# Kernel optimization log

Hardware: AMD Instinct MI355X
Metric: run time of the kernel (lower is better)

Reference implementation:

```python
import jax, jax.numpy as jnp
import numpy as np

N_NODES = 100000
N_EDGES = 1600000
D = 128
NUM_GRAPHS = 256


def setup_inputs() -> dict:
    key = jax.random.key(0)
    ks = jax.random.split(key, 8)
    x = jax.random.normal(ks[0], (N_NODES, D), dtype=jnp.float32)
    edge_index = jax.random.randint(ks[1], (2, N_EDGES), 0, N_NODES, dtype=jnp.int32)
    edge_attr = jax.random.normal(ks[2], (N_EDGES, D), dtype=jnp.float32) * 0.1
    batch = jnp.sort(jax.random.randint(ks[3], (N_NODES,), 0, NUM_GRAPHS, dtype=jnp.int32))
    primary = jax.random.randint(ks[4], (N_NODES,), 0, 2, dtype=jnp.int32)  # 1=primary, 0=condition
    scale = 1.0 / np.sqrt(D)
    W1 = jax.random.normal(ks[5], (D, D), dtype=jnp.float32) * scale
    b1 = jnp.zeros((D,), dtype=jnp.float32)
    W2 = jax.random.normal(ks[6], (D, D), dtype=jnp.float32) * scale
    b2 = jnp.zeros((D,), dtype=jnp.float32)
    return {"x": x, "edge_index": edge_index, "edge_attr": edge_attr,
            "batch": batch, "primary": primary,
            "W1": W1, "b1": b1, "W2": W2, "b2": b2}


def reference(x, edge_index, edge_attr, batch, primary, W1, b1, W2, b2):
    n = x.shape[0]
    # --- GIN-style GNN layer: node_rep = MLP(x + sum_{e:(s->d)} (x[s] + e_attr)) ---
    src, dst = edge_index[0], edge_index[1]
    msg = x[src] + edge_attr                                  # [E, D] gather (memory-bound)
    agg = jax.ops.segment_sum(msg, dst, num_segments=n)       # [N, D] scatter-add
    h = jax.nn.relu((x + agg) @ W1 + b1) @ W2 + b2            # [N, D]

    # --- per-graph mean pool over condition nodes (primary == 0) ---
    cond = (primary == 0)
    condf = cond.astype(h.dtype)[:, None]
    csum = jax.ops.segment_sum(h * condf, batch, num_segments=NUM_GRAPHS)   # [G, D]
    ccnt = jax.ops.segment_sum(condf, batch, num_segments=NUM_GRAPHS)       # [G, 1]
    # graphs with no condition nodes get a zero pool (matches torch branch)
    pool = jnp.where(ccnt > 0, csum / jnp.maximum(ccnt, 1.0), 0.0)          # [G, D]

    # --- assemble rows: per graph, primary rows [h | cond_pool] first, then zero rows
    # for condition nodes (matches the torch concat order) ---
    key = batch * 2 + cond.astype(batch.dtype)      # primary nodes sort before condition nodes
    order = jnp.argsort(key, stable=True)
    h_o = h[order]                                   # [N, D]
    pool_o = pool[batch[order]]                      # [N, D]
    prim_o = (primary[order] == 1)[:, None]
    out = jnp.where(prim_o, jnp.concatenate([h_o, pool_o], axis=1), 0.0)    # [N, 2D]
    return out
```

## Files before the change

kernel.cpp:

```cpp
#include <hip/hip_runtime.h>

#define D 128
#define NG 256

typedef __attribute__((ext_vector_type(8))) short bf16x8;
typedef __attribute__((ext_vector_type(4))) float f32x4;
typedef __attribute__((ext_vector_type(4))) float f4;
typedef __attribute__((ext_vector_type(2))) int i2;
typedef __attribute__((ext_vector_type(4))) ushort u16x4;

__device__ inline ushort f2bf(float f) {
  uint b = __float_as_uint(f);
  return (ushort)((b + 0x7fffu + ((b >> 16) & 1u)) >> 16);
}
__device__ inline float bf2f(ushort u) { return __uint_as_float((uint)u << 16); }

__global__ __launch_bounds__(256) void deg_counts_kernel(const int* __restrict__ ei,
                                                         int* __restrict__ deg,
                                                         const int* __restrict__ batch,
                                                         const int* __restrict__ primary,
                                                         int* __restrict__ ncount,
                                                         int* __restrict__ ccnt, int E, int N) {
  int e = blockIdx.x * blockDim.x + threadIdx.x;
  if (e < E) {
    int d = __builtin_nontemporal_load(&ei[E + e]);
    atomicAdd(&deg[d], 1);
  }
  if (e < N) {
    int g = batch[e];
    atomicAdd(&ncount[g], 1);
    if (primary[e] == 0) atomicAdd(&ccnt[g], 1);
  }
}

__global__ __launch_bounds__(256) void scan_block_sums(const int* __restrict__ deg,
                                                       int* __restrict__ bsum, int N) {
  __shared__ int red[256];
  int t = threadIdx.x;
  int base = blockIdx.x * 1024;
  int s = 0;
#pragma unroll
  for (int j = 0; j < 4; ++j) {
    int i = base + t * 4 + j;
    if (i < N) s += deg[i];
  }
  red[t] = s;
  __syncthreads();
  for (int o = 128; o > 0; o >>= 1) {
    if (t < o) red[t] += red[t + o];
    __syncthreads();
  }
  if (t == 0) bsum[blockIdx.x] = red[0];
}

__global__ void scan_bsum(int* __restrict__ bsum, int nb) {
  if (threadIdx.x == 0) {
    int run = 0;
    for (int i = 0; i < nb; ++i) {
      int v = bsum[i];
      bsum[i] = run;
      run += v;
    }
  }
}

__global__ __launch_bounds__(256) void scan_final(const int* __restrict__ deg,
                                                  const int* __restrict__ bsum,
                                                  int* __restrict__ off, int N) {
  __shared__ int ts[256];
  int t = threadIdx.x;
  int base = blockIdx.x * 1024;
  int v[4];
  int s = 0;
#pragma unroll
  for (int j = 0; j < 4; ++j) {
    int i = base + t * 4 + j;
    v[j] = (i < N) ? deg[i] : 0;
    s += v[j];
  }
  ts[t] = s;
  __syncthreads();
  for (int o = 1; o < 256; o <<= 1) {
    int u = (t >= o) ? ts[t - o] : 0;
    __syncthreads();
    ts[t] += u;
    __syncthreads();
  }
  int excl = ts[t] - s + bsum[blockIdx.x];
#pragma unroll
  for (int j = 0; j < 4; ++j) {
    int i = base + t * 4 + j;
    if (i < N) off[i] = excl;
    excl += v[j];
    if (i == N - 1) off[N] = excl;
  }
}

__global__ __launch_bounds__(256) void fill_kernel(const int* __restrict__ ei,
                                                   const int* __restrict__ off,
                                                   int* __restrict__ cursor,
                                                   i2* __restrict__ csr, int E) {
  int e = blockIdx.x * blockDim.x + threadIdx.x;
  if (e >= E) return;
  int s = __builtin_nontemporal_load(&ei[e]);
  int d = __builtin_nontemporal_load(&ei[E + e]);
  int slot = atomicAdd(&cursor[d], 1);
  i2 v;
  v.x = s;
  v.y = e;
  __builtin_nontemporal_store(v, &csr[off[d] + slot]);
}

__global__ __launch_bounds__(256) void cvt_kernel(const float* __restrict__ x,
                                                  ushort* __restrict__ xb,
                                                  const float* __restrict__ W1,
                                                  const float* __restrict__ W2,
                                                  ushort* __restrict__ W1T,
                                                  ushort* __restrict__ W2T, int total4) {
  int i = blockIdx.x * blockDim.x + threadIdx.x;
  if (i < total4) {
    f4 v = __builtin_nontemporal_load(&((const f4*)x)[i]);
    u16x4 o;
    o.x = f2bf(v.x);
    o.y = f2bf(v.y);
    o.z = f2bf(v.z);
    o.w = f2bf(v.w);
    ((u16x4*)xb)[i] = o;
  }
  if (i < 2 * D * D) {
    int w = i >> 14;
    int k = (i >> 7) & 127;
    int n = i & 127;
    const float* src = w ? W2 : W1;
    ushort* dst = w ? W2T : W1T;
    dst[n * 128 + k] = f2bf(src[k * 128 + n]);
  }
}

__global__ __launch_bounds__(256) void gather_kernel(const ushort* __restrict__ xb,
                                                     const float* __restrict__ ea,
                                                     const i2* __restrict__ csr,
                                                     const int* __restrict__ off,
                                                     ushort* __restrict__ yb, int N) {
  long long tid = (long long)blockIdx.x * blockDim.x + threadIdx.x;
  int n = (int)(tid >> 5);
  int c = (int)(tid & 31);
  if (n >= N) return;
  const f4* ea4 = (const f4*)ea;
  const u16x4* xb4 = (const u16x4*)xb;
  u16x4 self = xb4[(size_t)n * 32 + c];
  f4 acc;
  acc.x = bf2f(self.x);
  acc.y = bf2f(self.y);
  acc.z = bf2f(self.z);
  acc.w = bf2f(self.w);
  int s = off[n], e = off[n + 1];
  int k = s;
  for (; k + 4 <= e; k += 4) {
    i2 p0 = __builtin_nontemporal_load(&csr[k]);
    i2 p1 = __builtin_nontemporal_load(&csr[k + 1]);
    i2 p2 = __builtin_nontemporal_load(&csr[k + 2]);
    i2 p3 = __builtin_nontemporal_load(&csr[k + 3]);
    f4 a0 = __builtin_nontemporal_load(&ea4[(size_t)p0.y * 32 + c]);
    f4 a1 = __builtin_nontemporal_load(&ea4[(size_t)p1.y * 32 + c]);
    f4 a2 = __builtin_nontemporal_load(&ea4[(size_t)p2.y * 32 + c]);
    f4 a3 = __builtin_nontemporal_load(&ea4[(size_t)p3.y * 32 + c]);
    u16x4 u0 = xb4[(size_t)p0.x * 32 + c];
    u16x4 u1 = xb4[(size_t)p1.x * 32 + c];
    u16x4 u2 = xb4[(size_t)p2.x * 32 + c];
    u16x4 u3 = xb4[(size_t)p3.x * 32 + c];
    acc.x += (a0.x + bf2f(u0.x)) + (a1.x + bf2f(u1.x));
    acc.y += (a0.y + bf2f(u0.y)) + (a1.y + bf2f(u1.y));
    acc.z += (a0.z + bf2f(u0.z)) + (a1.z + bf2f(u1.z));
    acc.w += (a0.w + bf2f(u0.w)) + (a1.w + bf2f(u1.w));
    acc.x += (a2.x + bf2f(u2.x)) + (a3.x + bf2f(u3.x));
    acc.y += (a2.y + bf2f(u2.y)) + (a3.y + bf2f(u3.y));
    acc.z += (a2.z + bf2f(u2.z)) + (a3.z + bf2f(u3.z));
    acc.w += (a2.w + bf2f(u2.w)) + (a3.w + bf2f(u3.w));
  }
  for (; k < e; ++k) {
    i2 p0 = __builtin_nontemporal_load(&csr[k]);
    f4 a0 = __builtin_nontemporal_load(&ea4[(size_t)p0.y * 32 + c]);
    u16x4 u0 = xb4[(size_t)p0.x * 32 + c];
    acc.x += a0.x + bf2f(u0.x);
    acc.y += a0.y + bf2f(u0.y);
    acc.z += a0.z + bf2f(u0.z);
    acc.w += a0.w + bf2f(u0.w);
  }
  u16x4 o;
  o.x = f2bf(acc.x);
  o.y = f2bf(acc.y);
  o.z = f2bf(acc.z);
  o.w = f2bf(acc.w);
  __builtin_nontemporal_store(o, &((u16x4*)yb)[(size_t)n * 32 + c]);
}

__global__ void scan_kernel(const int* __restrict__ ncount, int* __restrict__ gstart) {
  __shared__ int a[NG];
  int tx = threadIdx.x;
  int v = ncount[tx];
  a[tx] = v;
  __syncthreads();
  for (int off = 1; off < NG; off <<= 1) {
    int u = (tx >= off) ? a[tx - off] : 0;
    __syncthreads();
    a[tx] += u;
    __syncthreads();
  }
  gstart[tx] = a[tx] - v;
  if (tx == NG - 1) gstart[NG] = a[tx];
}

__global__ __launch_bounds__(256) void rank_kernel(const int* __restrict__ primary,
                                                   const int* __restrict__ gstart,
                                                   const int* __restrict__ ccnt,
                                                   int* __restrict__ pos) {
  int g = blockIdx.x;
  int s = gstart[g], e = gstart[g + 1];
  int pcnt = (e - s) - ccnt[g];
  __shared__ int wcntP[4], wcntC[4];
  int prun = 0, crun = 0;
  for (int i0 = s; i0 < e; i0 += 256) {
    int n = i0 + threadIdx.x;
    bool valid = n < e;
    int isP = (valid && primary[n] == 1) ? 1 : 0;
    int isC = (valid && primary[n] != 1) ? 1 : 0;
    unsigned long long mP = __ballot(isP);
    unsigned long long mC = __ballot(isC);
    int lane = threadIdx.x & 63;
    int wid = threadIdx.x >> 6;
    if (lane == 0) { wcntP[wid] = __popcll(mP); wcntC[wid] = __popcll(mC); }
    __syncthreads();
    int preP = __popcll(mP & ((1ULL << lane) - 1ULL));
    int preC = __popcll(mC & ((1ULL << lane) - 1ULL));
    int woffP = 0, woffC = 0;
#pragma unroll
    for (int ww = 0; ww < 4; ++ww)
      if (ww < wid) { woffP += wcntP[ww]; woffC += wcntC[ww]; }
    int totP = wcntP[0] + wcntP[1] + wcntP[2] + wcntP[3];
    int totC = wcntC[0] + wcntC[1] + wcntC[2] + wcntC[3];
    if (valid) {
      if (isP)
        pos[n] = s + prun + woffP + preP;
      else
        pos[n] = ~(s + pcnt + crun + woffC + preC);
    }
    prun += totP;
    crun += totC;
    __syncthreads();
  }
}

__global__ __launch_bounds__(256) void mlp_mfma_kernel(
    const ushort* __restrict__ yb, float* __restrict__ out,
    const ushort* __restrict__ W1T, const float* __restrict__ b1,
    const ushort* __restrict__ W2T, const float* __restrict__ b2,
    const int* __restrict__ batch, const int* __restrict__ primary,
    const int* __restrict__ pos, float* __restrict__ csum, int N) {
  __shared__ ushort tl[4][16][D];
  __shared__ float csl[4][D];
  const int tid = threadIdx.x;
  const int w = tid >> 6;
  const int l = tid & 63;
  const int lr = l & 15;
  const int lg = l >> 4;
  const int base = blockIdx.x * 64;
  const int m0 = base + w * 16;

  for (int i = tid; i < 4 * D; i += 256) ((float*)csl)[i] = 0.f;
  int gmin = batch[base < N ? base : N - 1];
  __syncthreads();

  f32x4 acc[8];
#pragma unroll
  for (int t = 0; t < 8; ++t) {
    float bv = b1[t * 16 + lr];
    acc[t][0] = bv; acc[t][1] = bv; acc[t][2] = bv; acc[t][3] = bv;
  }
  int arow = m0 + lr;
  if (arow >= N) arow = N - 1;
#pragma unroll
  for (int kk = 0; kk < 4; ++kk) {
    bf16x8 a = *(const bf16x8*)&yb[(size_t)arow * D + kk * 32 + lg * 8];
#pragma unroll
    for (int t = 0; t < 8; ++t) {
      bf16x8 b = *(const bf16x8*)&W1T[(size_t)(t * 16 + lr) * D + kk * 32 + lg * 8];
      acc[t] = __builtin_amdgcn_mfma_f32_16x16x32_bf16(a, b, acc[t], 0, 0, 0);
    }
  }
#pragma unroll
  for (int t = 0; t < 8; ++t) {
#pragma unroll
    for (int r = 0; r < 4; ++r) {
      float v = acc[t][r];
      v = v > 0.f ? v : 0.f;
      int m = lg * 4 + r;
      int col = (t * 16 + lr) ^ ((m & 7) << 3);
      tl[w][m][col] = f2bf(v);
    }
  }
  __syncthreads();

  f32x4 acc2[8];
#pragma unroll
  for (int t = 0; t < 8; ++t) {
    float bv = b2[t * 16 + lr];
    acc2[t][0] = bv; acc2[t][1] = bv; acc2[t][2] = bv; acc2[t][3] = bv;
  }
#pragma unroll
  for (int kk = 0; kk < 4; ++kk) {
    bf16x8 a = *(const bf16x8*)&tl[w][lr][(kk * 32 + lg * 8) ^ ((lr & 7) << 3)];
#pragma unroll
    for (int t = 0; t < 8; ++t) {
      bf16x8 b = *(const bf16x8*)&W2T[(size_t)(t * 16 + lr) * D + kk * 32 + lg * 8];
      acc2[t] = __builtin_amdgcn_mfma_f32_16x16x32_bf16(a, b, acc2[t], 0, 0, 0);
    }
  }

#pragma unroll
  for (int r = 0; r < 4; ++r) {
    int m = m0 + lg * 4 + r;
    if (m >= N) continue;
    int p = pos[m];
    if (p >= 0) {
      size_t ro = (size_t)p * 256;
#pragma unroll
      for (int t = 0; t < 8; ++t)
        __builtin_nontemporal_store(acc2[t][r], &out[ro + t * 16 + lr]);
    } else {
      size_t ro = (size_t)(~p) * 256;
#pragma unroll
      for (int t = 0; t < 8; ++t) {
        __builtin_nontemporal_store(0.0f, &out[ro + t * 16 + lr]);
        __builtin_nontemporal_store(0.0f, &out[ro + 128 + t * 16 + lr]);
      }
      int g = batch[m];
      int gl = g - gmin;
      if (gl < 4) {
#pragma unroll
        for (int t = 0; t < 8; ++t) atomicAdd(&csl[gl][t * 16 + lr], acc2[t][r]);
      } else {
#pragma unroll
        for (int t = 0; t < 8; ++t)
          unsafeAtomicAdd(&csum[(size_t)g * D + t * 16 + lr], acc2[t][r]);
      }
    }
  }
  __syncthreads();
  for (int i = tid; i < 4 * D; i += 256) {
    float v = ((float*)csl)[i];
    if (v != 0.f) {
      int gl = i >> 7, c = i & 127;
      unsafeAtomicAdd(&csum[(size_t)(gmin + gl) * D + c], v);
    }
  }
}

__global__ __launch_bounds__(256) void poolwrite_kernel(const float* __restrict__ csum,
                                                        const int* __restrict__ ccnt,
                                                        const int* __restrict__ batch,
                                                        const int* __restrict__ pos,
                                                        float* __restrict__ out, int N) {
  long long tid = (long long)blockIdx.x * blockDim.x + threadIdx.x;
  int n = (int)(tid >> 5);
  int c = (int)(tid & 31);
  if (n >= N) return;
  int p = pos[n];
  if (p < 0) return;
  int g = batch[n];
  int cnt = ccnt[g];
  f4 v = {0.f, 0.f, 0.f, 0.f};
  if (cnt > 0) {
    f4 s4 = ((const f4*)csum)[(size_t)g * 32 + c];
    float inv = 1.0f / (float)cnt;
    v = s4 * inv;
  }
  __builtin_nontemporal_store(v, &((f4*)out)[(size_t)p * 64 + 32 + c]);
}

extern "C" void kernel_launch(void* const* d_in, const int* in_sizes, int n_in,
                              void* d_out, int out_size, void* d_ws, size_t ws_size,
                              hipStream_t stream) {
  const float* x = (const float*)d_in[0];
  const int* ei = (const int*)d_in[1];
  const float* ea = (const float*)d_in[2];
  const int* batch = (const int*)d_in[3];
  const int* primary = (const int*)d_in[4];
  const float* W1 = (const float*)d_in[5];
  const float* b1 = (const float*)d_in[6];
  const float* W2 = (const float*)d_in[7];
  const float* b2 = (const float*)d_in[8];
  float* out = (float*)d_out;

  const int N = in_sizes[0] / D;
  const int E = in_sizes[1] / 2;
  const int nb = (N + 1023) / 1024;

  float* csum = (float*)d_ws;
  ushort* yb = (ushort*)(csum + (size_t)NG * D);
  ushort* xb = yb + (size_t)N * D;
  ushort* W1T = xb + (size_t)N * D;
  ushort* W2T = W1T + D * D;
  i2* csr = (i2*)(W2T + D * D);
  int* ip = (int*)(csr + (size_t)E);
  int* deg = ip;
  int* off = deg + N;
  int* cursor = off + N + 4;
  int* bsum = cursor + N;
  int* ccnt = bsum + 128;
  int* ncount = ccnt + NG;
  int* gstart = ncount + NG;
  int* pos = gstart + 260;

  hipMemsetAsync(csum, 0, (size_t)NG * D * 4, stream);
  hipMemsetAsync(deg, 0, (size_t)N * 4, stream);
  hipMemsetAsync(cursor, 0, (size_t)N * 4, stream);
  hipMemsetAsync(ccnt, 0, (size_t)NG * 2 * 4, stream);

  deg_counts_kernel<<<(E + 255) / 256, 256, 0, stream>>>(ei, deg, batch, primary, ncount, ccnt,
                                                         E, N);
  scan_block_sums<<<nb, 256, 0, stream>>>(deg, bsum, N);
  scan_bsum<<<1, 64, 0, stream>>>(bsum, nb);
  scan_final<<<nb, 256, 0, stream>>>(deg, bsum, off, N);
  fill_kernel<<<(E + 255) / 256, 256, 0, stream>>>(ei, off, cursor, csr, E);
  cvt_kernel<<<((N * D / 4) + 255) / 256, 256, 0, stream>>>(x, xb, W1, W2, W1T, W2T, N * D / 4);
  {
    long long threads = (long long)N * 32;
    gather_kernel<<<(int)((threads + 255) / 256), 256, 0, stream>>>(xb, ea, csr, off, yb, N);
  }
  scan_kernel<<<1, NG, 0, stream>>>(ncount, gstart);
  rank_kernel<<<NG, 256, 0, stream>>>(primary, gstart, ccnt, pos);
  mlp_mfma_kernel<<<(N + 63) / 64, 256, 0, stream>>>(yb, out, W1T, b1, W2T, b2, batch, primary,
                                                     pos, csum, N);
  poolwrite_kernel<<<(int)(((long long)N * 32 + 255) / 256), 256, 0, stream>>>(csum, ccnt, batch,
                                                                               pos, out, N);
}
```

Before: 648.2 us.

## Fuse prep kernels, parallelize block-sum scan, split edge gather across half-waves

```diff
diff --git a/kernel.cpp b/kernel.cpp
--- a/kernel.cpp
+++ b/kernel.cpp
@@ -15,21 +15,33 @@
 }
 __device__ inline float bf2f(ushort u) { return __uint_as_float((uint)u << 16); }
 
-__global__ __launch_bounds__(256) void deg_counts_kernel(const int* __restrict__ ei,
-                                                         int* __restrict__ deg,
-                                                         const int* __restrict__ batch,
-                                                         const int* __restrict__ primary,
-                                                         int* __restrict__ ncount,
-                                                         int* __restrict__ ccnt, int E, int N) {
-  int e = blockIdx.x * blockDim.x + threadIdx.x;
-  if (e < E) {
-    int d = __builtin_nontemporal_load(&ei[E + e]);
-    atomicAdd(&deg[d], 1);
-  }
-  if (e < N) {
-    int g = batch[e];
+__global__ __launch_bounds__(256) void prep_kernel(
+    const int* __restrict__ ei, int* __restrict__ deg,
+    const int* __restrict__ batch, const int* __restrict__ primary,
+    int* __restrict__ ncount, int* __restrict__ ccnt,
+    const float* __restrict__ x, ushort* __restrict__ xb,
+    const float* __restrict__ W1, const float* __restrict__ W2,
+    ushort* __restrict__ W1T, ushort* __restrict__ W2T, int E, int N, int total4) {
+  int i = blockIdx.x * blockDim.x + threadIdx.x;
+  if (i < E) atomicAdd(&deg[ei[E + i]], 1);
+  if (i < N) {
+    int g = batch[i];
     atomicAdd(&ncount[g], 1);
-    if (primary[e] == 0) atomicAdd(&ccnt[g], 1);
+    if (primary[i] == 0) atomicAdd(&ccnt[g], 1);
+  }
+  if (i < total4) {
+    f4 v = __builtin_nontemporal_load(&((const f4*)x)[i]);
+    u16x4 o;
+    o.x = f2bf(v.x); o.y = f2bf(v.y); o.z = f2bf(v.z); o.w = f2bf(v.w);
+    ((u16x4*)xb)[i] = o;
+  }
+  if (i < 2 * D * D) {
+    int w = i >> 14;
+    int k = (i >> 7) & 127;
+    int n = i & 127;
+    const float* src = w ? W2 : W1;
+    ushort* dst = w ? W2T : W1T;
+    dst[n * 128 + k] = f2bf(src[k * 128 + n]);
   }
 }
 
@@ -54,14 +66,18 @@
 }
 
 __global__ void scan_bsum(int* __restrict__ bsum, int nb) {
-  if (threadIdx.x == 0) {
-    int run = 0;
-    for (int i = 0; i < nb; ++i) {
-      int v = bsum[i];
-      bsum[i] = run;
-      run += v;
-    }
-  }
+  __shared__ int a[128];
+  int t = threadIdx.x;
+  int v = (t < nb) ? bsum[t] : 0;
+  a[t] = v;
+  __syncthreads();
+  for (int o = 1; o < 128; o <<= 1) {
+    int u = (t >= o) ? a[t - o] : 0;
+    __syncthreads();
+    a[t] += u;
+    __syncthreads();
+  }
+  if (t < nb) bsum[t] = a[t] - v;
 }
 
 __global__ __launch_bounds__(256) void scan_final(const int* __restrict__ deg,
@@ -102,97 +118,91 @@
                                                    i2* __restrict__ csr, int E) {
   int e = blockIdx.x * blockDim.x + threadIdx.x;
   if (e >= E) return;
-  int s = __builtin_nontemporal_load(&ei[e]);
-  int d = __builtin_nontemporal_load(&ei[E + e]);
+  int s = ei[e];
+  int d = ei[E + e];
   int slot = atomicAdd(&cursor[d], 1);
   i2 v;
   v.x = s;
   v.y = e;
-  __builtin_nontemporal_store(v, &csr[off[d] + slot]);
-}
-
-__global__ __launch_bounds__(256) void cvt_kernel(const float* __restrict__ x,
-                                                  ushort* __restrict__ xb,
-                                                  const float* __restrict__ W1,
-                                                  const float* __restrict__ W2,
-                                                  ushort* __restrict__ W1T,
-                                                  ushort* __restrict__ W2T, int total4) {
-  int i = blockIdx.x * blockDim.x + threadIdx.x;
-  if (i < total4) {
-    f4 v = __builtin_nontemporal_load(&((const f4*)x)[i]);
-    u16x4 o;
-    o.x = f2bf(v.x);
-    o.y = f2bf(v.y);
-    o.z = f2bf(v.z);
-    o.w = f2bf(v.w);
-    ((u16x4*)xb)[i] = o;
-  }
-  if (i < 2 * D * D) {
-    int w = i >> 14;
-    int k = (i >> 7) & 127;
-    int n = i & 127;
-    const float* src = w ? W2 : W1;
-    ushort* dst = w ? W2T : W1T;
-    dst[n * 128 + k] = f2bf(src[k * 128 + n]);
-  }
-}
-
-__global__ __launch_bounds__(256) void gather_kernel(const ushort* __restrict__ xb,
-                                                     const float* __restrict__ ea,
-                                                     const i2* __restrict__ csr,
-                                                     const int* __restrict__ off,
-                                                     ushort* __restrict__ yb, int N) {
-  long long tid = (long long)blockIdx.x * blockDim.x + threadIdx.x;
-  int n = (int)(tid >> 5);
-  int c = (int)(tid & 31);
-  if (n >= N) return;
+  csr[off[d] + slot] = v;
+}
+
+__global__ __launch_bounds__(256, 8) void gather_kernel(const ushort* __restrict__ xb,
+                                                        const float* __restrict__ ea,
+                                                        const i2* __restrict__ csr,
+                                                        const int* __restrict__ off,
+                                                        ushort* __restrict__ yb, int N) {
+  const int lane = threadIdx.x & 63;
+  const int h = lane >> 5;
+  const int c = lane & 31;
+  const int wave = (blockIdx.x * 256 + (threadIdx.x & ~63)) >> 6;
   const f4* ea4 = (const f4*)ea;
   const u16x4* xb4 = (const u16x4*)xb;
-  u16x4 self = xb4[(size_t)n * 32 + c];
-  f4 acc;
-  acc.x = bf2f(self.x);
-  acc.y = bf2f(self.y);
-  acc.z = bf2f(self.z);
-  acc.w = bf2f(self.w);
-  int s = off[n], e = off[n + 1];
-  int k = s;
-  for (; k + 4 <= e; k += 4) {
-    i2 p0 = __builtin_nontemporal_load(&csr[k]);
-    i2 p1 = __builtin_nontemporal_load(&csr[k + 1]);
-    i2 p2 = __builtin_nontemporal_load(&csr[k + 2]);
-    i2 p3 = __builtin_nontemporal_load(&csr[k + 3]);
-    f4 a0 = __builtin_nontemporal_load(&ea4[(size_t)p0.y * 32 + c]);
-    f4 a1 = __builtin_nontemporal_load(&ea4[(size_t)p1.y * 32 + c]);
-    f4 a2 = __builtin_nontemporal_load(&ea4[(size_t)p2.y * 32 + c]);
-    f4 a3 = __builtin_nontemporal_load(&ea4[(size_t)p3.y * 32 + c]);
-    u16x4 u0 = xb4[(size_t)p0.x * 32 + c];
-    u16x4 u1 = xb4[(size_t)p1.x * 32 + c];
-    u16x4 u2 = xb4[(size_t)p2.x * 32 + c];
-    u16x4 u3 = xb4[(size_t)p3.x * 32 + c];
-    acc.x += (a0.x + bf2f(u0.x)) + (a1.x + bf2f(u1.x));
-    acc.y += (a0.y + bf2f(u0.y)) + (a1.y + bf2f(u1.y));
-    acc.z += (a0.z + bf2f(u0.z)) + (a1.z + bf2f(u1.z));
-    acc.w += (a0.w + bf2f(u0.w)) + (a1.w + bf2f(u1.w));
-    acc.x += (a2.x + bf2f(u2.x)) + (a3.x + bf2f(u3.x));
-    acc.y += (a2.y + bf2f(u2.y)) + (a3.y + bf2f(u3.y));
-    acc.z += (a2.z + bf2f(u2.z)) + (a3.z + bf2f(u3.z));
-    acc.w += (a2.w + bf2f(u2.w)) + (a3.w + bf2f(u3.w));
-  }
-  for (; k < e; ++k) {
-    i2 p0 = __builtin_nontemporal_load(&csr[k]);
-    f4 a0 = __builtin_nontemporal_load(&ea4[(size_t)p0.y * 32 + c]);
-    u16x4 u0 = xb4[(size_t)p0.x * 32 + c];
-    acc.x += a0.x + bf2f(u0.x);
-    acc.y += a0.y + bf2f(u0.y);
-    acc.z += a0.z + bf2f(u0.z);
-    acc.w += a0.w + bf2f(u0.w);
-  }
-  u16x4 o;
-  o.x = f2bf(acc.x);
-  o.y = f2bf(acc.y);
-  o.z = f2bf(acc.z);
-  o.w = f2bf(acc.w);
-  __builtin_nontemporal_store(o, &((u16x4*)yb)[(size_t)n * 32 + c]);
+  const int row0 = wave * 4;
+#pragma unroll 1
+  for (int r = 0; r < 4; ++r) {
+    const int n = row0 + r;
+    if (n >= N) return;
+    f4 acc = {0.f, 0.f, 0.f, 0.f};
+    int k = off[n];
+    const int e = off[n + 1];
+#pragma unroll 1
+    for (; k + 8 <= e; k += 8) {
+      i2 p0 = csr[k + h];
+      i2 p1 = csr[k + 2 + h];
+      i2 p2 = csr[k + 4 + h];
+      i2 p3 = csr[k + 6 + h];
+      f4 a0 = __builtin_nontemporal_load(&ea4[(size_t)p0.y * 32 + c]);
+      f4 a1 = __builtin_nontemporal_load(&ea4[(size_t)p1.y * 32 + c]);
+      f4 a2 = __builtin_nontemporal_load(&ea4[(size_t)p2.y * 32 + c]);
+      f4 a3 = __builtin_nontemporal_load(&ea4[(size_t)p3.y * 32 + c]);
+      u16x4 u0 = xb4[(size_t)p0.x * 32 + c];
+      u16x4 u1 = xb4[(size_t)p1.x * 32 + c];
+      u16x4 u2 = xb4[(size_t)p2.x * 32 + c];
+      u16x4 u3 = xb4[(size_t)p3.x * 32 + c];
+      acc.x += (a0.x + bf2f(u0.x)) + (a1.x + bf2f(u1.x));
+      acc.y += (a0.y + bf2f(u0.y)) + (a1.y + bf2f(u1.y));
+      acc.z += (a0.z + bf2f(u0.z)) + (a1.z + bf2f(u1.z));
+      acc.w += (a0.w + bf2f(u0.w)) + (a1.w + bf2f(u1.w));
+      acc.x += (a2.x + bf2f(u2.x)) + (a3.x + bf2f(u3.x));
+      acc.y += (a2.y + bf2f(u2.y)) + (a3.y + bf2f(u3.y));
+      acc.z += (a2.z + bf2f(u2.z)) + (a3.z + bf2f(u3.z));
+      acc.w += (a2.w + bf2f(u2.w)) + (a3.w + bf2f(u3.w));
+    }
+#pragma unroll 1
+    for (; k + 2 <= e; k += 2) {
+      i2 p0 = csr[k + h];
+      f4 a0 = __builtin_nontemporal_load(&ea4[(size_t)p0.y * 32 + c]);
+      u16x4 u0 = xb4[(size_t)p0.x * 32 + c];
+      acc.x += a0.x + bf2f(u0.x);
+      acc.y += a0.y + bf2f(u0.y);
+      acc.z += a0.z + bf2f(u0.z);
+      acc.w += a0.w + bf2f(u0.w);
+    }
+    if (k + h < e) {
+      i2 p0 = csr[k + h];
+      f4 a0 = __builtin_nontemporal_load(&ea4[(size_t)p0.y * 32 + c]);
+      u16x4 u0 = xb4[(size_t)p0.x * 32 + c];
+      acc.x += a0.x + bf2f(u0.x);
+      acc.y += a0.y + bf2f(u0.y);
+      acc.z += a0.z + bf2f(u0.z);
+      acc.w += a0.w + bf2f(u0.w);
+    }
+    acc.x += __shfl_xor(acc.x, 32, 64);
+    acc.y += __shfl_xor(acc.y, 32, 64);
+    acc.z += __shfl_xor(acc.z, 32, 64);
+    acc.w += __shfl_xor(acc.w, 32, 64);
+    if (h == 0) {
+      u16x4 self = xb4[(size_t)n * 32 + c];
+      acc.x += bf2f(self.x);
+      acc.y += bf2f(self.y);
+      acc.z += bf2f(self.z);
+      acc.w += bf2f(self.w);
+      u16x4 o;
+      o.x = f2bf(acc.x); o.y = f2bf(acc.y); o.z = f2bf(acc.z); o.w = f2bf(acc.w);
+      __builtin_nontemporal_store(o, &((u16x4*)yb)[(size_t)n * 32 + c]);
+    }
+  }
 }
 
 __global__ void scan_kernel(const int* __restrict__ ncount, int* __restrict__ gstart) {
@@ -395,6 +405,7 @@
   const int N = in_sizes[0] / D;
   const int E = in_sizes[1] / 2;
   const int nb = (N + 1023) / 1024;
+  const int total4 = N * D / 4;
 
   float* csum = (float*)d_ws;
   ushort* yb = (ushort*)(csum + (size_t)NG * D);
@@ -417,19 +428,19 @@
   hipMemsetAsync(cursor, 0, (size_t)N * 4, stream);
   hipMemsetAsync(ccnt, 0, (size_t)NG * 2 * 4, stream);
 
-  deg_counts_kernel<<<(E + 255) / 256, 256, 0, stream>>>(ei, deg, batch, primary, ncount, ccnt,
-                                                         E, N);
+  prep_kernel<<<(total4 + 255) / 256, 256, 0, stream>>>(ei, deg, batch, primary, ncount, ccnt,
+                                                        x, xb, W1, W2, W1T, W2T, E, N, total4);
   scan_block_sums<<<nb, 256, 0, stream>>>(deg, bsum, N);
-  scan_bsum<<<1, 64, 0, stream>>>(bsum, nb);
+  scan_bsum<<<1, 128, 0, stream>>>(bsum, nb);
   scan_final<<<nb, 256, 0, stream>>>(deg, bsum, off, N);
   fill_kernel<<<(E + 255) / 256, 256, 0, stream>>>(ei, off, cursor, csr, E);
-  cvt_kernel<<<((N * D / 4) + 255) / 256, 256, 0, stream>>>(x, xb, W1, W2, W1T, W2T, N * D / 4);
-  {
-    long long threads = (long long)N * 32;
-    gather_kernel<<<(int)((threads + 255) / 256), 256, 0, stream>>>(xb, ea, csr, off, yb, N);
-  }
   scan_kernel<<<1, NG, 0, stream>>>(ncount, gstart);
   rank_kernel<<<NG, 256, 0, stream>>>(primary, gstart, ccnt, pos);
+  {
+    int waves = (N + 3) / 4;
+    int blocks = (waves + 3) / 4;
+    gather_kernel<<<blocks, 256, 0, stream>>>(xb, ea, csr, off, yb, N);
+  }
   mlp_mfma_kernel<<<(N + 63) / 64, 256, 0, stream>>>(yb, out, W1T, b1, W2T, b2, batch, primary,
                                                      pos, csum, N);
   poolwrite_kernel<<<(int)(((long long)N * 32 + 255) / 256), 256, 0, stream>>>(csum, ccnt, batch,
```

Result: no change. 638.1 us (-1.6%).
